# Kernel optimization log

Hardware: AMD Instinct MI355X
Metric: run time of the kernel (lower is better)

Reference implementation:

```python
import jax, jax.numpy as jnp
import numpy as np

N_HEADS = 8
NEG_INF = -1e30  # finite stand-in for -inf in masked_fill (exact 0 prob after softmax)


def apply_rotary_emb(x, cos, sin):
    # x: [B, H, T, hd]; cos/sin: [T, hd] -> broadcast over B, H
    d = x.shape[-1]
    x1, x2 = x[..., : d // 2], x[..., d // 2 :]
    x_rot = jnp.concatenate((-x2, x1), axis=-1)
    return x * cos[None, None] + x_rot * sin[None, None]


def setup_inputs() -> dict:
    key = jax.random.key(0)
    ks = jax.random.split(key, 5)
    B, T, C, hd = 4, 2048, 512, 64
    x = jax.random.normal(ks[0], (B, T, C), dtype=jnp.float32)
    cos = jax.random.uniform(ks[1], (T, hd), dtype=jnp.float32)
    sin = jax.random.uniform(ks[2], (T, hd), dtype=jnp.float32)
    # xavier_uniform-ish scale for linear weights
    W_qkv = jax.random.normal(ks[3], (3 * C, C), dtype=jnp.float32) * (1.0 / np.sqrt(C))
    W_out = jax.random.normal(ks[4], (C, C), dtype=jnp.float32) * (1.0 / np.sqrt(C))
    return {"x": x, "cos": cos, "sin": sin, "W_qkv": W_qkv, "W_out": W_out}


def reference(x, cos, sin, W_qkv, W_out):
    B, T, C = x.shape
    H = N_HEADS
    hd = C // H
    # qkv projection (torch Linear: y = x @ W^T), split into q, k, v as [B, H, T, hd]
    qkv = (x @ W_qkv.T).reshape(B, T, 3, H, hd)
    qkv = jnp.transpose(qkv, (2, 0, 3, 1, 4))
    q, k, v = qkv[0], qkv[1], qkv[2]
    # RoPE on q, k
    q = apply_rotary_emb(q, cos[:T], sin[:T])
    k = apply_rotary_emb(k, cos[:T], sin[:T])
    scale = jnp.sqrt(jnp.float32(hd))
    attn = jnp.einsum("bhqd,bhkd->bhqk", q, k) / scale  # [B, H, T, T]
    causal = jnp.tril(jnp.ones((T, T), dtype=bool))
    attn = jnp.where(causal[None, None], attn, NEG_INF)
    attn = jax.nn.softmax(attn, axis=-1)
    out = jnp.einsum("bhqk,bhkd->bhqd", attn, v)  # [B, H, T, hd]
    out = jnp.transpose(out, (0, 2, 1, 3)).reshape(B, T, C)
    return out @ W_out.T
```

## Files before the change

kernel.cpp:

```cpp
#include <hip/hip_runtime.h>
#include <hip/hip_bf16.h>
#include <math.h>

#define B_SZ 4
#define T_SZ 2048
#define C_SZ 512
#define H_SZ 8
#define HD 64
#define QSCALE 0.1803368801111137f

typedef __bf16 bf16;
typedef __bf16 bf16x8 __attribute__((ext_vector_type(8)));
typedef float f32x4 __attribute__((ext_vector_type(4)));

__device__ __forceinline__ f32x4 mfma16(bf16x8 a, bf16x8 b, f32x4 c) {
    return __builtin_amdgcn_mfma_f32_16x16x32_bf16(a, b, c, 0, 0, 0);
}

#define GLD_LDS16(g, l) __builtin_amdgcn_global_load_lds( \
    (__attribute__((address_space(1))) void*)(void*)(g),  \
    (__attribute__((address_space(3))) void*)(l), 16, 0, 0)

__global__ __launch_bounds__(256) void cvt_all(
    const float* __restrict__ x, const float* __restrict__ wqkv,
    const float* __restrict__ wout, bf16* __restrict__ xb,
    bf16* __restrict__ wqb, bf16* __restrict__ wob) {
  int i = blockIdx.x * 256 + threadIdx.x;
  const int n0 = (B_SZ*T_SZ*C_SZ)/4, n1 = (3*C_SZ*C_SZ)/4, n2 = (C_SZ*C_SZ)/4;
  const float4* s; bf16* d; int j;
  if (i < n0)                { s = (const float4*)x;    d = xb;  j = i; }
  else if (i < n0 + n1)      { s = (const float4*)wqkv; d = wqb; j = i - n0; }
  else if (i < n0 + n1 + n2) { s = (const float4*)wout; d = wob; j = i - n0 - n1; }
  else return;
  float4 v = s[j];
  union { bf16 h[4]; uint2 u; } p;
  p.h[0] = (bf16)v.x; p.h[1] = (bf16)v.y; p.h[2] = (bf16)v.z; p.h[3] = (bf16)v.w;
  *(uint2*)(d + (size_t)j * 4) = p.u;
}

__global__ __launch_bounds__(256) void gemm_qkv(
    const bf16* __restrict__ A, const bf16* __restrict__ Bw,
    const float* __restrict__ cp, const float* __restrict__ sp,
    bf16* __restrict__ oq, bf16* __restrict__ ok, bf16* __restrict__ ov) {
  __shared__ bf16 sA[128 * 32];
  __shared__ bf16 sB[128 * 32];
  const int tid = threadIdx.x;
  const int m0 = blockIdx.x * 128, n0 = blockIdx.y * 128;
  const int w = tid >> 6, lane = tid & 63, quad = lane >> 4, l16 = lane & 15;
  const int wm = (w >> 1) * 64, wn = (w & 1) * 64;
  const int srow = tid >> 2, scol = (tid & 3) * 8;
  const int K = C_SZ;
  f32x4 acc[4][4] = {};
  for (int k0 = 0; k0 < K; k0 += 32) {
    __syncthreads();
    const bf16* ga = A  + (size_t)(m0 + srow) * K + k0 + scol;
    const bf16* gb = Bw + (size_t)(n0 + srow) * K + k0 + scol;
    GLD_LDS16(ga,                 sA + tid * 8);
    GLD_LDS16(ga + (size_t)64*K,  sA + tid * 8 + 2048);
    GLD_LDS16(gb,                 sB + tid * 8);
    GLD_LDS16(gb + (size_t)64*K,  sB + tid * 8 + 2048);
    __syncthreads();
    bf16x8 af[4], bfr[4];
#pragma unroll
    for (int i = 0; i < 4; i++)
      af[i] = *(const bf16x8*)(sA + (wm + i*16 + l16) * 32 + quad * 8);
#pragma unroll
    for (int j = 0; j < 4; j++)
      bfr[j] = *(const bf16x8*)(sB + (wn + j*16 + l16) * 32 + quad * 8);
#pragma unroll
    for (int i = 0; i < 4; i++)
#pragma unroll
      for (int j = 0; j < 4; j++)
        acc[i][j] = mfma16(af[i], bfr[j], acc[i][j]);
  }
  const int three = n0 >> 9;
  if (three < 2) {
    bf16* dst0 = three == 0 ? oq : ok;
#pragma unroll
    for (int i = 0; i < 4; i++)
#pragma unroll
      for (int r = 0; r < 4; r++) {
        const int m = m0 + wm + i*16 + quad*4 + r;
        const int b = m >> 11, t = m & (T_SZ - 1);
#pragma unroll
        for (int j = 0; j < 2; j++) {
          const int dcol = j*16 + l16;
          const int h = ((n0 & 511) + wn + dcol) >> 6;
          const float c1 = cp[t*HD + dcol],     s1 = sp[t*HD + dcol];
          const float c2 = cp[t*HD + dcol + 32], s2 = sp[t*HD + dcol + 32];
          const float a = acc[i][j][r], bb = acc[i][j+2][r];
          float o1 = a * c1 - bb * s1;
          float o2 = bb * c2 + a * s2;
          if (three == 0) { o1 *= QSCALE; o2 *= QSCALE; }
          bf16* dst = dst0 + (((size_t)(b*H_SZ + h)) * T_SZ + t) * HD;
          dst[dcol]      = (bf16)o1;
          dst[dcol + 32] = (bf16)o2;
        }
      }
  } else {
#pragma unroll
    for (int i = 0; i < 4; i++)
#pragma unroll
      for (int j = 0; j < 4; j++) {
        const int n = n0 + wn + j*16 + l16;
        const int h = (n & 511) >> 6, dcol = n & 63;
#pragma unroll
        for (int r = 0; r < 4; r++) {
          const int m = m0 + wm + i*16 + quad*4 + r;
          const int b = m >> 11, t = m & (T_SZ - 1);
          ov[(((size_t)(b*H_SZ + h)) * HD + dcol) * T_SZ + t] = (bf16)acc[i][j][r];
        }
      }
  }
}

__global__ __launch_bounds__(256) void gemm_out(
    const bf16* __restrict__ A, const bf16* __restrict__ Bw,
    float* __restrict__ dst) {
  __shared__ bf16 sA[64 * 32];
  __shared__ bf16 sB[128 * 32];
  const int tid = threadIdx.x;
  const int m0 = blockIdx.x * 64, n0 = blockIdx.y * 128;
  const int w = tid >> 6, lane = tid & 63, quad = lane >> 4, l16 = lane & 15;
  const int wm = (w & 1) * 32, wn = (w >> 1) * 64;
  const int srow = tid >> 2, scol = (tid & 3) * 8;
  const int K = C_SZ;
  f32x4 acc[2][4] = {};
  for (int k0 = 0; k0 < K; k0 += 32) {
    __syncthreads();
    const bf16* ga = A  + (size_t)(m0 + srow) * K + k0 + scol;
    const bf16* gb = Bw + (size_t)(n0 + srow) * K + k0 + scol;
    GLD_LDS16(ga,                 sA + tid * 8);
    GLD_LDS16(gb,                 sB + tid * 8);
    GLD_LDS16(gb + (size_t)64*K,  sB + tid * 8 + 2048);
    __syncthreads();
    bf16x8 af[2], bfr[4];
#pragma unroll
    for (int i = 0; i < 2; i++)
      af[i] = *(const bf16x8*)(sA + (wm + i*16 + l16) * 32 + quad * 8);
#pragma unroll
    for (int j = 0; j < 4; j++)
      bfr[j] = *(const bf16x8*)(sB + (wn + j*16 + l16) * 32 + quad * 8);
#pragma unroll
    for (int i = 0; i < 2; i++)
#pragma unroll
      for (int j = 0; j < 4; j++)
        acc[i][j] = mfma16(af[i], bfr[j], acc[i][j]);
  }
#pragma unroll
  for (int i = 0; i < 2; i++)
#pragma unroll
    for (int j = 0; j < 4; j++)
#pragma unroll
      for (int r = 0; r < 4; r++) {
        const int m = m0 + wm + i*16 + quad*4 + r;
        const int n = n0 + wn + j*16 + l16;
        dst[(size_t)m * C_SZ + n] = acc[i][j][r];
      }
}

__device__ __forceinline__ int tile_of(int g) {
  int qi = (int)((sqrtf((float)g + 1.f) - 1.f) * 0.5f);
  while (4 * (qi + 1) * (qi + 2) <= g) ++qi;
  while (4 * qi * (qi + 1) > g) --qi;
  return qi;
}

__global__ __launch_bounds__(256, 3) void flash_attn(
    const bf16* __restrict__ qb, const bf16* __restrict__ kb,
    const bf16* __restrict__ vtb, bf16* __restrict__ Oa,
    float* __restrict__ lbuf) {
  __shared__ bf16 sK[2][32 * 64];
  __shared__ bf16 sVT[2][64 * 32];
  __shared__ bf16 sP[4][2560];
  const int tid = threadIdx.x, w = tid >> 6, lane = tid & 63;
  const int quad = lane >> 4, l16 = lane & 15;
  const int bh = blockIdx.x & 31;
  const int p  = blockIdx.x >> 5;
  const int gs = 12 * p, ge = gs + 12;
  int qi = tile_of(gs);
  int tend = 4 * (qi + 1) * (qi + 2);
  int q0w = qi * 256 + w * 64;
  const bf16* Q  = qb  + (size_t)bh * T_SZ * HD;
  const bf16* Kp = kb  + (size_t)bh * T_SZ * HD;
  const bf16* Vt = vtb + (size_t)bh * HD * T_SZ;
  bf16x8 qf[4][2];
#pragma unroll
  for (int nt = 0; nt < 4; nt++)
#pragma unroll
    for (int ds = 0; ds < 2; ds++)
      qf[nt][ds] = *(const bf16x8*)(Q + (size_t)(q0w + nt*16 + l16) * HD + ds*32 + quad*8);
  float l_[4] = {0.f, 0.f, 0.f, 0.f};
  f32x4 ot[4][4] = {};
  bf16* sPw = &sP[w][0];
  const int srow = tid >> 3, scg = (tid & 7) ^ (srow & 7);
  const int vrow = tid >> 2, vcg = (tid & 3) ^ (vrow & 3);

  auto partial_epilogue = [&]() {
    const int pf = (qi * (qi + 1)) / 3;
    const int rec = (bh * 8 + qi) * 6 + (p - pf);
#pragma unroll
    for (int nt = 0; nt < 4; nt++) {
      float s = l_[nt];
      s += __shfl_xor(s, 16);
      s += __shfl_xor(s, 32);
      if (quad == 0) lbuf[rec * 256 + w*64 + nt*16 + l16] = s;
    }
#pragma unroll
    for (int h = 0; h < 2; h++) {
      asm volatile("" ::: "memory");
#pragma unroll
      for (int dt = 0; dt < 4; dt++)
#pragma unroll
        for (int n2 = 0; n2 < 2; n2++) {
          const int nt = h*2 + n2;
          union { bf16 h4[4]; unsigned long long ull; } pk;
#pragma unroll
          for (int r = 0; r < 4; r++) pk.h4[r] = (bf16)ot[dt][nt][r];
          *(unsigned long long*)(sPw + (n2*16 + l16)*72 + dt*16 + quad*4) = pk.ull;
        }
      asm volatile("" ::: "memory");
      const int oq = lane >> 1, hf = lane & 1;
      bf16* dst = Oa + (size_t)rec * 16384 + (w*64 + h*32 + oq) * 64 + hf * 32;
#pragma unroll
      for (int j = 0; j < 4; j++)
        *(uint4*)(dst + j*8) = *(const uint4*)(sPw + oq*72 + hf*32 + j*8);
    }
    asm volatile("" ::: "memory");
  };

  {
    const int kt0 = (gs - 4*qi*(qi+1)) * 32;
    GLD_LDS16(Kp + (size_t)(kt0 + srow) * HD + scg*8, sK[gs & 1]  + tid*8);
    GLD_LDS16(Vt + (size_t)vrow * T_SZ + kt0 + vcg*8, sVT[gs & 1] + tid*8);
  }

  for (int g = gs; g < ge; g++) {
    const int kt = (g - 4*qi*(qi+1)) * 32;
    __syncthreads();
    if (g + 1 < ge) {
      const int qn = (g + 1 >= tend) ? qi + 1 : qi;
      const int kn = (g + 1 - 4*qn*(qn+1)) * 32;
      GLD_LDS16(Kp + (size_t)(kn + srow) * HD + scg*8, sK[(g+1) & 1]  + tid*8);
      GLD_LDS16(Vt + (size_t)vrow * T_SZ + kn + vcg*8, sVT[(g+1) & 1] + tid*8);
    }
    if (kt <= q0w + 63) {
      const bf16* cK = sK[g & 1];
      const bf16* cV = sVT[g & 1];
      f32x4 st[2][4] = {};
#pragma unroll
      for (int mt = 0; mt < 2; mt++) {
#pragma unroll
        for (int ds = 0; ds < 2; ds++) {
          const int row = mt*16 + l16, cl = ds*4 + quad;
          const bf16x8 kf = *(const bf16x8*)(cK + row*64 + (cl ^ (row & 7)) * 8);
#pragma unroll
          for (int nt = 0; nt < 4; nt++)
            st[mt][nt] = mfma16(kf, qf[nt][ds], st[mt][nt]);
        }
      }
      if (kt + 31 > q0w) {
#pragma unroll
        for (int nt = 0; nt < 4; nt++) {
          const int qg = q0w + nt*16 + l16;
          const int kb0 = kt + quad*4;
#pragma unroll
          for (int mt = 0; mt < 2; mt++)
#pragma unroll
            for (int r = 0; r < 4; r++)
              st[mt][nt][r] = (kb0 + mt*16 + r <= qg) ? st[mt][nt][r] : -1e30f;
        }
      }
#pragma unroll
      for (int nt = 0; nt < 4; nt++) {
        float sum = 0.f;
#pragma unroll
        for (int mt = 0; mt < 2; mt++) {
          union { bf16 h4[4]; unsigned long long ull; } pk;
#pragma unroll
          for (int r = 0; r < 4; r++) {
            const float pv = __builtin_amdgcn_exp2f(st[mt][nt][r]);
            sum += pv;
            pk.h4[r] = (bf16)pv;
          }
          *(unsigned long long*)(sPw + (nt*16 + l16)*40 + mt*16 + quad*4) = pk.ull;
        }
        l_[nt] += sum;
      }
      asm volatile("" ::: "memory");
      bf16x8 pfr[4];
#pragma unroll
      for (int nt = 0; nt < 4; nt++)
        pfr[nt] = *(const bf16x8*)(sPw + (nt*16 + l16)*40 + quad*8);
#pragma unroll
      for (int dt = 0; dt < 4; dt++) {
        const int row = dt*16 + l16;
        const bf16x8 vf = *(const bf16x8*)(cV + row*32 + (quad ^ (row & 3)) * 8);
#pragma unroll
        for (int nt = 0; nt < 4; nt++)
          ot[dt][nt] = mfma16(vf, pfr[nt], ot[dt][nt]);
      }
    }
    if (g + 1 == tend || g + 1 == ge) {
      partial_epilogue();
      if (g + 1 == tend && g + 1 < ge) {
        qi++; tend = 4 * (qi + 1) * (qi + 2); q0w = qi * 256 + w * 64;
#pragma unroll
        for (int nt = 0; nt < 4; nt++)
#pragma unroll
          for (int ds = 0; ds < 2; ds++)
            qf[nt][ds] = *(const bf16x8*)(Q + (size_t)(q0w + nt*16 + l16) * HD + ds*32 + quad*8);
#pragma unroll
        for (int nt = 0; nt < 4; nt++) l_[nt] = 0.f;
#pragma unroll
        for (int dt = 0; dt < 4; dt++)
#pragma unroll
          for (int nt = 0; nt < 4; nt++)
            ot[dt][nt] = f32x4{0.f, 0.f, 0.f, 0.f};
      }
    }
  }
}

__global__ __launch_bounds__(256) void combine_o(
    const bf16* __restrict__ Oa, const float* __restrict__ lbuf,
    bf16* __restrict__ ao) {
  const int inst = blockIdx.x;
  const int bh = inst & 31, qi = inst >> 5;
  const int b = bh >> 3, h = bh & 7;
  const int g0 = 4 * qi * (qi + 1), gL = g0 + 8*qi + 7;
  const int pf = g0 / 12, pl = gL / 12;
  const int n = pl - pf + 1;
  const int base = (bh * 8 + qi) * 6;
  const int q = threadIdx.x;
  float l = 0.f;
  for (int s = 0; s < n; s++) l += lbuf[(base + s) * 256 + q];
  const float inv = 1.f / l;
  float acc[64] = {};
  for (int s = 0; s < n; s++) {
    const bf16* ps = Oa + ((size_t)(base + s)) * 16384 + q * 64;
#pragma unroll
    for (int c = 0; c < 8; c++) {
      union { uint4 u; bf16 h8[8]; } a;
      a.u = *(const uint4*)(ps + c*8);
#pragma unroll
      for (int j = 0; j < 8; j++) acc[c*8 + j] += (float)a.h8[j];
    }
  }
  const int tg = qi * 256 + q;
  bf16* dst = ao + ((size_t)(b*T_SZ + tg)) * C_SZ + h*HD;
#pragma unroll
  for (int c = 0; c < 8; c++) {
    union { uint4 u; bf16 h8[8]; } o;
#pragma unroll
    for (int j = 0; j < 8; j++) o.h8[j] = (bf16)(acc[c*8 + j] * inv);
    *(uint4*)(dst + c*8) = o.u;
  }
}

extern "C" void kernel_launch(void* const* d_in, const int* in_sizes, int n_in,
                              void* d_out, int out_size, void* d_ws, size_t ws_size,
                              hipStream_t stream) {
  const float* x    = (const float*)d_in[0];
  const float* cosp = (const float*)d_in[1];
  const float* sinp = (const float*)d_in[2];
  const float* wqkv = (const float*)d_in[3];
  const float* wout = (const float*)d_in[4];
  char* ws = (char*)d_ws;
  bf16* xb    = (bf16*)(ws);
  bf16* wqkvb = (bf16*)(ws +  8388608);
  bf16* woutb = (bf16*)(ws +  9961472);
  bf16* qbuf  = (bf16*)(ws + 10485760);
  bf16* kbuf  = (bf16*)(ws + 18874368);
  bf16* vtbuf = (bf16*)(ws + 27262976);
  bf16* ao    = (bf16*)(ws + 35651584);
  bf16* Oa    = (bf16*)(ws + 44040192);
  float* lbuf = (float*)(ws + 94371840);

  cvt_all<<<dim3(5120), dim3(256), 0, stream>>>(x, wqkv, wout, xb, wqkvb, woutb);
  gemm_qkv<<<dim3(64, 12), dim3(256), 0, stream>>>(
      xb, wqkvb, cosp, sinp, qbuf, kbuf, vtbuf);
  flash_attn<<<dim3(768), dim3(256), 0, stream>>>(qbuf, kbuf, vtbuf, Oa, lbuf);
  combine_o<<<dim3(256), dim3(256), 0, stream>>>(Oa, lbuf, ao);
  gemm_out<<<dim3(128, 4), dim3(256), 0, stream>>>(ao, woutb, (float*)d_out);
}
```

Baseline: 166.2 us.

## Split attention work per wave with independent 64-query tiles and direct global K/V loads

Reworks the split-K flash attention so each wave owns its own segment of 8 key tiles over 64-query tiles, rather than a block sharing 256-query tiles. The shared-LDS double-buffered K/V staging and __syncthreads are removed, and each wave loads K and V fragments straight from global memory into registers. The aim is finer load balancing across the causal triangle, no wasted fully-masked tiles, and no block-level barriers. In exchange, K/V are no longer shared across waves through LDS, so global traffic rises, and there are more partial records for combine_o to reduce, which now also uses more threads per query.

```diff
diff --git a/kernel.cpp b/kernel.cpp
--- a/kernel.cpp
+++ b/kernel.cpp
@@ -160,27 +160,26 @@
 }
 
 __device__ __forceinline__ int tile_of(int g) {
-  int qi = (int)((sqrtf((float)g + 1.f) - 1.f) * 0.5f);
-  while (4 * (qi + 1) * (qi + 2) <= g) ++qi;
-  while (4 * qi * (qi + 1) > g) --qi;
-  return qi;
-}
-
-__global__ __launch_bounds__(256, 3) void flash_attn(
+  int j = (int)((sqrtf(4.f*(float)g + 1.f) - 1.f) * 0.5f);
+  while ((j + 1) * (j + 2) <= g) ++j;
+  while (j * (j + 1) > g) --j;
+  return j;
+}
+
+__global__ __launch_bounds__(256) void flash_attn(
     const bf16* __restrict__ qb, const bf16* __restrict__ kb,
     const bf16* __restrict__ vtb, bf16* __restrict__ Oa,
     float* __restrict__ lbuf) {
-  __shared__ bf16 sK[2][32 * 64];
-  __shared__ bf16 sVT[2][64 * 32];
   __shared__ bf16 sP[4][2560];
   const int tid = threadIdx.x, w = tid >> 6, lane = tid & 63;
   const int quad = lane >> 4, l16 = lane & 15;
   const int bh = blockIdx.x & 31;
-  const int p  = blockIdx.x >> 5;
-  const int gs = 12 * p, ge = gs + 12;
-  int qi = tile_of(gs);
-  int tend = 4 * (qi + 1) * (qi + 2);
-  int q0w = qi * 256 + w * 64;
+  const int sgrp = blockIdx.x >> 5;
+  const int seg = sgrp * 4 + w;
+  const int gs = seg * 8, ge = gs + 8;
+  int j = tile_of(gs);
+  int tend = (j + 1) * (j + 2);
+  int q0 = j * 64;
   const bf16* Q  = qb  + (size_t)bh * T_SZ * HD;
   const bf16* Kp = kb  + (size_t)bh * T_SZ * HD;
   const bf16* Vt = vtb + (size_t)bh * HD * T_SZ;
@@ -189,22 +188,19 @@
   for (int nt = 0; nt < 4; nt++)
 #pragma unroll
     for (int ds = 0; ds < 2; ds++)
-      qf[nt][ds] = *(const bf16x8*)(Q + (size_t)(q0w + nt*16 + l16) * HD + ds*32 + quad*8);
+      qf[nt][ds] = *(const bf16x8*)(Q + (size_t)(q0 + nt*16 + l16) * HD + ds*32 + quad*8);
   float l_[4] = {0.f, 0.f, 0.f, 0.f};
   f32x4 ot[4][4] = {};
   bf16* sPw = &sP[w][0];
-  const int srow = tid >> 3, scg = (tid & 7) ^ (srow & 7);
-  const int vrow = tid >> 2, vcg = (tid & 3) ^ (vrow & 3);
-
-  auto partial_epilogue = [&]() {
-    const int pf = (qi * (qi + 1)) / 3;
-    const int rec = (bh * 8 + qi) * 6 + (p - pf);
+
+  auto emit = [&]() {
+    const int rec = (bh * 32 + j) * 10 + (seg - ((j * (j + 1)) >> 3));
 #pragma unroll
     for (int nt = 0; nt < 4; nt++) {
       float s = l_[nt];
       s += __shfl_xor(s, 16);
       s += __shfl_xor(s, 32);
-      if (quad == 0) lbuf[rec * 256 + w*64 + nt*16 + l16] = s;
+      if (quad == 0) lbuf[rec * 64 + nt*16 + l16] = s;
     }
 #pragma unroll
     for (int h = 0; h < 2; h++) {
@@ -221,95 +217,83 @@
         }
       asm volatile("" ::: "memory");
       const int oq = lane >> 1, hf = lane & 1;
-      bf16* dst = Oa + (size_t)rec * 16384 + (w*64 + h*32 + oq) * 64 + hf * 32;
-#pragma unroll
-      for (int j = 0; j < 4; j++)
-        *(uint4*)(dst + j*8) = *(const uint4*)(sPw + oq*72 + hf*32 + j*8);
+      bf16* dst = Oa + (size_t)rec * 4096 + (h*32 + oq) * 64 + hf * 32;
+#pragma unroll
+      for (int c = 0; c < 4; c++)
+        *(uint4*)(dst + c*8) = *(const uint4*)(sPw + oq*72 + hf*32 + c*8);
     }
     asm volatile("" ::: "memory");
   };
 
-  {
-    const int kt0 = (gs - 4*qi*(qi+1)) * 32;
-    GLD_LDS16(Kp + (size_t)(kt0 + srow) * HD + scg*8, sK[gs & 1]  + tid*8);
-    GLD_LDS16(Vt + (size_t)vrow * T_SZ + kt0 + vcg*8, sVT[gs & 1] + tid*8);
-  }
-
   for (int g = gs; g < ge; g++) {
-    const int kt = (g - 4*qi*(qi+1)) * 32;
-    __syncthreads();
-    if (g + 1 < ge) {
-      const int qn = (g + 1 >= tend) ? qi + 1 : qi;
-      const int kn = (g + 1 - 4*qn*(qn+1)) * 32;
-      GLD_LDS16(Kp + (size_t)(kn + srow) * HD + scg*8, sK[(g+1) & 1]  + tid*8);
-      GLD_LDS16(Vt + (size_t)vrow * T_SZ + kn + vcg*8, sVT[(g+1) & 1] + tid*8);
-    }
-    if (kt <= q0w + 63) {
-      const bf16* cK = sK[g & 1];
-      const bf16* cV = sVT[g & 1];
-      f32x4 st[2][4] = {};
+    const int kt = (g - j * (j + 1)) * 32;
+    const bf16* kbase = Kp + (size_t)(kt + l16) * HD + quad * 8;
+    bf16x8 kf[2][2];
+#pragma unroll
+    for (int mt = 0; mt < 2; mt++)
+#pragma unroll
+      for (int ds = 0; ds < 2; ds++)
+        kf[mt][ds] = *(const bf16x8*)(kbase + mt*16*HD + ds*32);
+    const bf16* vbase = Vt + (size_t)l16 * T_SZ + kt + quad * 8;
+    bf16x8 vf[4];
+#pragma unroll
+    for (int dt = 0; dt < 4; dt++)
+      vf[dt] = *(const bf16x8*)(vbase + (size_t)dt*16*T_SZ);
+    f32x4 st[2][4] = {};
+#pragma unroll
+    for (int mt = 0; mt < 2; mt++)
+#pragma unroll
+      for (int ds = 0; ds < 2; ds++)
+#pragma unroll
+        for (int nt = 0; nt < 4; nt++)
+          st[mt][nt] = mfma16(kf[mt][ds], qf[nt][ds], st[mt][nt]);
+    if (kt + 31 > q0) {
+#pragma unroll
+      for (int nt = 0; nt < 4; nt++) {
+        const int qg = q0 + nt*16 + l16;
+        const int kb0 = kt + quad*4;
+#pragma unroll
+        for (int mt = 0; mt < 2; mt++)
+#pragma unroll
+          for (int r = 0; r < 4; r++)
+            st[mt][nt][r] = (kb0 + mt*16 + r <= qg) ? st[mt][nt][r] : -1e30f;
+      }
+    }
+#pragma unroll
+    for (int nt = 0; nt < 4; nt++) {
+      float sum = 0.f;
 #pragma unroll
       for (int mt = 0; mt < 2; mt++) {
-#pragma unroll
-        for (int ds = 0; ds < 2; ds++) {
-          const int row = mt*16 + l16, cl = ds*4 + quad;
-          const bf16x8 kf = *(const bf16x8*)(cK + row*64 + (cl ^ (row & 7)) * 8);
-#pragma unroll
-          for (int nt = 0; nt < 4; nt++)
-            st[mt][nt] = mfma16(kf, qf[nt][ds], st[mt][nt]);
+        union { bf16 h4[4]; unsigned long long ull; } pk;
+#pragma unroll
+        for (int r = 0; r < 4; r++) {
+          const float pv = __builtin_amdgcn_exp2f(st[mt][nt][r]);
+          sum += pv;
+          pk.h4[r] = (bf16)pv;
         }
-      }
-      if (kt + 31 > q0w) {
-#pragma unroll
-        for (int nt = 0; nt < 4; nt++) {
-          const int qg = q0w + nt*16 + l16;
-          const int kb0 = kt + quad*4;
-#pragma unroll
-          for (int mt = 0; mt < 2; mt++)
-#pragma unroll
-            for (int r = 0; r < 4; r++)
-              st[mt][nt][r] = (kb0 + mt*16 + r <= qg) ? st[mt][nt][r] : -1e30f;
-        }
-      }
-#pragma unroll
-      for (int nt = 0; nt < 4; nt++) {
-        float sum = 0.f;
-#pragma unroll
-        for (int mt = 0; mt < 2; mt++) {
-          union { bf16 h4[4]; unsigned long long ull; } pk;
-#pragma unroll
-          for (int r = 0; r < 4; r++) {
-            const float pv = __builtin_amdgcn_exp2f(st[mt][nt][r]);
-            sum += pv;
-            pk.h4[r] = (bf16)pv;
-          }
-          *(unsigned long long*)(sPw + (nt*16 + l16)*40 + mt*16 + quad*4) = pk.ull;
-        }
-        l_[nt] += sum;
-      }
-      asm volatile("" ::: "memory");
-      bf16x8 pfr[4];
+        *(unsigned long long*)(sPw + (nt*16 + l16)*40 + mt*16 + quad*4) = pk.ull;
+      }
+      l_[nt] += sum;
+    }
+    asm volatile("" ::: "memory");
+    bf16x8 pfr[4];
+#pragma unroll
+    for (int nt = 0; nt < 4; nt++)
+      pfr[nt] = *(const bf16x8*)(sPw + (nt*16 + l16)*40 + quad*8);
+#pragma unroll
+    for (int dt = 0; dt < 4; dt++)
 #pragma unroll
       for (int nt = 0; nt < 4; nt++)
-        pfr[nt] = *(const bf16x8*)(sPw + (nt*16 + l16)*40 + quad*8);
-#pragma unroll
-      for (int dt = 0; dt < 4; dt++) {
-        const int row = dt*16 + l16;
-        const bf16x8 vf = *(const bf16x8*)(cV + row*32 + (quad ^ (row & 3)) * 8);
+        ot[dt][nt] = mfma16(vf[dt], pfr[nt], ot[dt][nt]);
+    if (g + 1 == tend) {
+      emit();
+      if (g + 1 < ge) {
+        j++; tend = (j + 1) * (j + 2); q0 = j * 64;
 #pragma unroll
         for (int nt = 0; nt < 4; nt++)
-          ot[dt][nt] = mfma16(vf, pfr[nt], ot[dt][nt]);
-      }
-    }
-    if (g + 1 == tend || g + 1 == ge) {
-      partial_epilogue();
-      if (g + 1 == tend && g + 1 < ge) {
-        qi++; tend = 4 * (qi + 1) * (qi + 2); q0w = qi * 256 + w * 64;
-#pragma unroll
-        for (int nt = 0; nt < 4; nt++)
 #pragma unroll
           for (int ds = 0; ds < 2; ds++)
-            qf[nt][ds] = *(const bf16x8*)(Q + (size_t)(q0w + nt*16 + l16) * HD + ds*32 + quad*8);
+            qf[nt][ds] = *(const bf16x8*)(Q + (size_t)(q0 + nt*16 + l16) * HD + ds*32 + quad*8);
 #pragma unroll
         for (int nt = 0; nt < 4; nt++) l_[nt] = 0.f;
 #pragma unroll
@@ -318,6 +302,8 @@
           for (int nt = 0; nt < 4; nt++)
             ot[dt][nt] = f32x4{0.f, 0.f, 0.f, 0.f};
       }
+    } else if (g + 1 == ge) {
+      emit();
     }
   }
 }
@@ -326,34 +312,35 @@
     const bf16* __restrict__ Oa, const float* __restrict__ lbuf,
     bf16* __restrict__ ao) {
   const int inst = blockIdx.x;
-  const int bh = inst & 31, qi = inst >> 5;
+  const int bh = inst & 31, j = inst >> 5;
   const int b = bh >> 3, h = bh & 7;
-  const int g0 = 4 * qi * (qi + 1), gL = g0 + 8*qi + 7;
-  const int pf = g0 / 12, pl = gL / 12;
+  const int g0 = j * (j + 1), gL = (j + 1) * (j + 2) - 1;
+  const int pf = g0 >> 3, pl = gL >> 3;
   const int n = pl - pf + 1;
-  const int base = (bh * 8 + qi) * 6;
-  const int q = threadIdx.x;
+  const int base = (bh * 32 + j) * 10;
+  const int t = threadIdx.x;
+  const int q = t >> 2, dg = (t & 3) * 16;
   float l = 0.f;
-  for (int s = 0; s < n; s++) l += lbuf[(base + s) * 256 + q];
+  for (int s = 0; s < n; s++) l += lbuf[(base + s) * 64 + q];
   const float inv = 1.f / l;
-  float acc[64] = {};
+  float acc[16] = {};
   for (int s = 0; s < n; s++) {
-    const bf16* ps = Oa + ((size_t)(base + s)) * 16384 + q * 64;
-#pragma unroll
-    for (int c = 0; c < 8; c++) {
+    const bf16* ps = Oa + ((size_t)(base + s)) * 4096 + q * 64 + dg;
+#pragma unroll
+    for (int c = 0; c < 2; c++) {
       union { uint4 u; bf16 h8[8]; } a;
       a.u = *(const uint4*)(ps + c*8);
 #pragma unroll
-      for (int j = 0; j < 8; j++) acc[c*8 + j] += (float)a.h8[j];
-    }
-  }
-  const int tg = qi * 256 + q;
-  bf16* dst = ao + ((size_t)(b*T_SZ + tg)) * C_SZ + h*HD;
-#pragma unroll
-  for (int c = 0; c < 8; c++) {
+      for (int k = 0; k < 8; k++) acc[c*8 + k] += (float)a.h8[k];
+    }
+  }
+  const int tg = j * 64 + q;
+  bf16* dst = ao + ((size_t)(b*T_SZ + tg)) * C_SZ + h*HD + dg;
+#pragma unroll
+  for (int c = 0; c < 2; c++) {
     union { uint4 u; bf16 h8[8]; } o;
 #pragma unroll
-    for (int j = 0; j < 8; j++) o.h8[j] = (bf16)(acc[c*8 + j] * inv);
+    for (int k = 0; k < 8; k++) o.h8[k] = (bf16)(acc[c*8 + k] * inv);
     *(uint4*)(dst + c*8) = o.u;
   }
 }
@@ -375,12 +362,12 @@
   bf16* vtbuf = (bf16*)(ws + 27262976);
   bf16* ao    = (bf16*)(ws + 35651584);
   bf16* Oa    = (bf16*)(ws + 44040192);
-  float* lbuf = (float*)(ws + 94371840);
+  float* lbuf = (float*)(ws + 127926272);
 
   cvt_all<<<dim3(5120), dim3(256), 0, stream>>>(x, wqkv, wout, xb, wqkvb, woutb);
   gemm_qkv<<<dim3(64, 12), dim3(256), 0, stream>>>(
       xb, wqkvb, cosp, sinp, qbuf, kbuf, vtbuf);
-  flash_attn<<<dim3(768), dim3(256), 0, stream>>>(qbuf, kbuf, vtbuf, Oa, lbuf);
-  combine_o<<<dim3(256), dim3(256), 0, stream>>>(Oa, lbuf, ao);
+  flash_attn<<<dim3(1056), dim3(256), 0, stream>>>(qbuf, kbuf, vtbuf, Oa, lbuf);
+  combine_o<<<dim3(1024), dim3(256), 0, stream>>>(Oa, lbuf, ao);
   gemm_out<<<dim3(128, 4), dim3(256), 0, stream>>>(ao, woutb, (float*)d_out);
 }
```

Result: slower. 175.9 us (+5.8%).
